# Kernel optimization log

Measured on AMD Instinct MI355X. Metric: run time of the kernel, lower is better.

The kernel has to match this reference:

```python
import jax, jax.numpy as jnp
import numpy as np

N_QUBITS = 8
HIDDEN_DIM = 128
GATE_FAMILIES = ("rx", "ry", "rz")


def _rx(theta):
    theta = jnp.asarray(theta)
    c = jnp.cos(theta / 2).astype(jnp.complex64)
    s = (-1j * jnp.sin(theta / 2)).astype(jnp.complex64)
    return jnp.stack([jnp.stack([c, s], -1), jnp.stack([s, c], -1)], -2)


def _ry(theta):
    theta = jnp.asarray(theta)
    c = jnp.cos(theta / 2).astype(jnp.complex64)
    s = jnp.sin(theta / 2).astype(jnp.complex64)
    return jnp.stack([jnp.stack([c, -s], -1), jnp.stack([s, c], -1)], -2)


def _rz(theta):
    theta = jnp.asarray(theta)
    em = jnp.exp(-0.5j * theta).astype(jnp.complex64)
    ep = jnp.exp(0.5j * theta).astype(jnp.complex64)
    z = jnp.zeros_like(em)
    return jnp.stack([jnp.stack([em, z], -1), jnp.stack([z, ep], -1)], -2)


_GATE = {"rx": _rx, "ry": _ry, "rz": _rz}


def _apply_1q(state, mat, wire, n):
    # state: (B, 2^n) complex; wire 0 is the most-significant bit (PennyLane convention)
    B = state.shape[0]
    L, R = 2 ** wire, 2 ** (n - 1 - wire)
    s = state.reshape(B, L, 2, R)
    if mat.ndim == 2:
        s = jnp.einsum("ij,bljr->blir", mat, s)
    else:  # per-sample angles -> (B,2,2) matrices
        s = jnp.einsum("bij,bljr->blir", mat, s)
    return s.reshape(B, 2 ** n)


def _apply_cnot(state, wire, n):
    # CNOT with control=wire, target=wire+1 (adjacent chain)
    B = state.shape[0]
    L, R = 2 ** wire, 2 ** (n - 2 - wire)
    s = state.reshape(B, L, 2, 2, R)
    s = jnp.concatenate([s[:, :, :1], s[:, :, 1:, ::-1]], axis=2)
    return s.reshape(B, 2 ** n)


def _circuit(x, params):
    # x: (B, n) data-encoding angles; params: (n,) trainable angles. Returns <Z_0>, shape (B,).
    B, n = x.shape
    state = jnp.zeros((B, 2 ** n), jnp.complex64).at[:, 0].set(1.0)
    for i in range(n):
        state = _apply_1q(state, _rx(x[:, i]), i, n)
    for i in range(n):
        mat = _GATE[GATE_FAMILIES[i % len(GATE_FAMILIES)]](params[i])
        state = _apply_1q(state, mat, i, n)
    for i in range(n - 1):
        state = _apply_cnot(state, i, n)
    probs = state.real ** 2 + state.imag ** 2
    p = probs.reshape(B, 2, -1).sum(-1)
    return p[:, 0] - p[:, 1]


def setup_inputs() -> dict:
    key = jax.random.key(0)
    ks = jax.random.split(key, 13)
    T, B, D, H, n = 256, 256, 128, HIDDEN_DIM, N_QUBITS
    scale = 1.0 / np.sqrt(D + H)
    inputs = jax.random.normal(ks[0], (T, B, D), jnp.float32)
    d = {"inputs": inputs}
    names = ["f", "i", "u", "o"]
    for j, nm in enumerate(names):
        d["W" + nm] = jax.random.normal(ks[1 + 3 * j], (n, D + H), jnp.float32) * scale
        d["b" + nm] = jax.random.normal(ks[2 + 3 * j], (n,), jnp.float32) * scale
        d["p" + nm] = jax.random.normal(ks[3 + 3 * j], (n,), jnp.float32)
    return d


def reference(inputs, Wf, bf, Wi, bi, Wu, bu, Wo, bo, pf, pi, pu, po):
    T, B, D = inputs.shape
    h0 = jnp.zeros((B, HIDDEN_DIM), inputs.dtype)
    c0 = jnp.zeros((B, HIDDEN_DIM), inputs.dtype)

    def step(carry, x):
        hx, cx = carry
        comb = jnp.concatenate([x, hx], axis=1)  # (B, D+H)
        f = jax.nn.sigmoid(_circuit(comb @ Wf.T + bf, pf))[:, None]
        ig = jax.nn.sigmoid(_circuit(comb @ Wi.T + bi, pi))[:, None]
        g = jnp.tanh(_circuit(comb @ Wu.T + bu, pu))[:, None]
        o = jax.nn.sigmoid(_circuit(comb @ Wo.T + bo, po))[:, None]
        cx = f * cx + ig * g
        hx = o * jnp.tanh(cx)
        return (hx, cx), hx

    (hx, cx), outs = jax.lax.scan(step, (h0, c0), inputs)
    return outs, hx, cx
```

## Files before the change

### kernel.cpp

```cpp
#include <hip/hip_runtime.h>

#define TT 256
#define BB 256
#define DD 128

__device__ __forceinline__ float rdlane(float v, int l) {
    return __int_as_float(__builtin_amdgcn_readlane(__float_as_int(v), l));
}
__device__ __forceinline__ float frcp(float x) { return __builtin_amdgcn_rcpf(x); }
__device__ __forceinline__ float fastcos(float z) {
    float r = z * 0.15915494309189535f;
    r = __builtin_amdgcn_fractf(r);
    return __builtin_amdgcn_cosf(r);
}

__global__ __launch_bounds__(256) void k_angles(
    const float* __restrict__ x,
    const float* __restrict__ Wf, const float* __restrict__ bf, const float* __restrict__ pf,
    const float* __restrict__ Wi, const float* __restrict__ bi, const float* __restrict__ pi,
    const float* __restrict__ Wu, const float* __restrict__ bu, const float* __restrict__ pu,
    const float* __restrict__ Wo, const float* __restrict__ bo, const float* __restrict__ po,
    float4* __restrict__ A)
{
    __shared__ float4 w4[4][32];
    float* w = reinterpret_cast<float*>(w4);
    int tid = threadIdx.x;
    for (int k = tid; k < 512; k += 256) {
        int g = k >> 7, j = k & 127;
        const float* W = (g == 0) ? Wf : (g == 1) ? Wi : (g == 2) ? Wu : Wo;
        w[g * 128 + j] = W[j];
    }
    __syncthreads();

    int r = blockIdx.x * 256 + tid;
    int t = r >> 8, b = r & 255;
    const float4* xr = reinterpret_cast<const float4*>(x + (size_t)r * DD);

    float af = bf[0] + pf[0];
    float ai = bi[0] + pi[0];
    float au = bu[0] + pu[0];
    float ao = bo[0] + po[0];
    #pragma unroll
    for (int k = 0; k < 32; ++k) {
        float4 v  = xr[k];
        float4 f4 = w4[0][k], i4 = w4[1][k], u4 = w4[2][k], o4 = w4[3][k];
        af = fmaf(v.x, f4.x, fmaf(v.y, f4.y, fmaf(v.z, f4.z, fmaf(v.w, f4.w, af))));
        ai = fmaf(v.x, i4.x, fmaf(v.y, i4.y, fmaf(v.z, i4.z, fmaf(v.w, i4.w, ai))));
        au = fmaf(v.x, u4.x, fmaf(v.y, u4.y, fmaf(v.z, u4.z, fmaf(v.w, u4.w, au))));
        ao = fmaf(v.x, o4.x, fmaf(v.y, o4.y, fmaf(v.z, o4.z, fmaf(v.w, o4.w, ao))));
    }
    A[b * TT + t] = make_float4(af, ai, au, ao);
}

__global__ __launch_bounds__(64) void k_recur(
    const float4* __restrict__ A,
    const float* __restrict__ Wf, const float* __restrict__ Wi,
    const float* __restrict__ Wu, const float* __restrict__ Wo,
    float* __restrict__ out)
{
    int b = blockIdx.x;
    int lane = threadIdx.x;
    __shared__ float As[4][260];

    #pragma unroll
    for (int k = 0; k < 4; ++k) {
        int t = lane + 64 * k;
        float4 a4 = A[b * TT + t];
        As[0][t] = a4.x; As[1][t] = a4.y; As[2][t] = a4.z; As[3][t] = a4.w;
    }

    int g = lane & 3;
    const float* W = (g == 0) ? Wf : (g == 1) ? Wi : (g == 2) ? Wu : Wo;
    const float4* W4 = reinterpret_cast<const float4*>(W + 128);
    float S = 0.f;
    #pragma unroll
    for (int k = 0; k < 32; ++k) {
        float4 v = W4[k];
        S += (v.x + v.y) + (v.z + v.w);
    }
    float kk   = (g == 2) ? -2.f : -1.f;
    float Aact = (g == 2) ?  2.f :  1.f;
    float Bact = (g == 2) ? -1.f :  0.f;

    __syncthreads();

    float c = 0.f, h = 0.f;
    float a_cur = As[g][0];
    float* outp = out + b * 128 + lane * 2;

    for (int t = 0; t < TT; ++t) {
        float a_next = As[g][t + 1];
        float z = fmaf(h, S, a_cur);
        float v = fastcos(z);
        float e = __expf(kk * v);
        float s = frcp(1.f + e);
        float act = fmaf(Aact, s, Bact);
        float fv = rdlane(act, 0);
        float iv = rdlane(act, 1);
        float uv = rdlane(act, 2);
        float ov = rdlane(act, 3);
        c = fmaf(fv, c, iv * uv);
        float e2 = __expf(2.f * c);
        float th = 1.f - 2.f * frcp(1.f + e2);
        h = ov * th;
        *reinterpret_cast<float2*>(outp + (size_t)t * (BB * 128)) = make_float2(h, h);
        a_cur = a_next;
    }
    float* hx = out + (size_t)TT * BB * 128;
    float* cx = hx + BB * 128;
    *reinterpret_cast<float2*>(hx + b * 128 + lane * 2) = make_float2(h, h);
    *reinterpret_cast<float2*>(cx + b * 128 + lane * 2) = make_float2(c, c);
}

extern "C" void kernel_launch(void* const* d_in, const int* in_sizes, int n_in,
                              void* d_out, int out_size, void* d_ws, size_t ws_size,
                              hipStream_t stream) {
    const float* x = (const float*)d_in[0];
    const float *Wf, *bf, *pf, *Wi, *bi, *pi, *Wu, *bu, *pu, *Wo, *bo, *po;
    if (n_in >= 13 && in_sizes[3] == 8 && in_sizes[4] == 2048) {
        Wf = (const float*)d_in[1];  bf = (const float*)d_in[2];  pf = (const float*)d_in[3];
        Wi = (const float*)d_in[4];  bi = (const float*)d_in[5];  pi = (const float*)d_in[6];
        Wu = (const float*)d_in[7];  bu = (const float*)d_in[8];  pu = (const float*)d_in[9];
        Wo = (const float*)d_in[10]; bo = (const float*)d_in[11]; po = (const float*)d_in[12];
    } else {
        Wf = (const float*)d_in[1];  bf = (const float*)d_in[2];
        Wi = (const float*)d_in[3];  bi = (const float*)d_in[4];
        Wu = (const float*)d_in[5];  bu = (const float*)d_in[6];
        Wo = (const float*)d_in[7];  bo = (const float*)d_in[8];
        pf = (const float*)d_in[9];  pi = (const float*)d_in[10];
        pu = (const float*)d_in[11]; po = (const float*)d_in[12];
    }
    float4* A = (float4*)d_ws;

    k_angles<<<dim3(256), dim3(256), 0, stream>>>(
        x, Wf, bf, pf, Wi, bi, pi, Wu, bu, pu, Wo, bo, po, A);
    k_recur<<<dim3(256), dim3(64), 0, stream>>>(
        A, Wf, Wi, Wu, Wo, (float*)d_out);
}
```

Baseline: 39.44 us.

## Run one batch row per thread in recurrence and expand outputs in separate kernel

The recurrence kernel now gives each thread a whole batch sample, computing all four gates itself instead of spreading them over four lanes and exchanging through readlane. It keeps the angle rows in a time-major layout with an 8-deep register prefetch, and writes the scalar h (and final c) back into the workspace. A new k_expand kernel then broadcasts those scalars into the full output with wide, coalesced float4 stores. The aim is to take the large strided output writes off the serial recurrence path. The cost is that only 4 blocks of 64 threads run the recurrence, so each thread carries a long dependent chain with little parallelism to hide latency.

```diff
diff --git a/kernel.cpp b/kernel.cpp
--- a/kernel.cpp
+++ b/kernel.cpp
@@ -4,15 +4,15 @@
 #define BB 256
 #define DD 128
 
-__device__ __forceinline__ float rdlane(float v, int l) {
-    return __int_as_float(__builtin_amdgcn_readlane(__float_as_int(v), l));
-}
 __device__ __forceinline__ float frcp(float x) { return __builtin_amdgcn_rcpf(x); }
 __device__ __forceinline__ float fastcos(float z) {
     float r = z * 0.15915494309189535f;
     r = __builtin_amdgcn_fractf(r);
     return __builtin_amdgcn_cosf(r);
 }
+#define C_SIG  (-1.4426950408889634f)
+#define C_TANH (-2.8853900817779268f)
+#define C_TC   ( 2.8853900817779268f)
 
 __global__ __launch_bounds__(256) void k_angles(
     const float* __restrict__ x,
@@ -33,7 +33,6 @@
     __syncthreads();
 
     int r = blockIdx.x * 256 + tid;
-    int t = r >> 8, b = r & 255;
     const float4* xr = reinterpret_cast<const float4*>(x + (size_t)r * DD);
 
     float af = bf[0] + pf[0];
@@ -49,67 +48,88 @@
         au = fmaf(v.x, u4.x, fmaf(v.y, u4.y, fmaf(v.z, u4.z, fmaf(v.w, u4.w, au))));
         ao = fmaf(v.x, o4.x, fmaf(v.y, o4.y, fmaf(v.z, o4.z, fmaf(v.w, o4.w, ao))));
     }
-    A[b * TT + t] = make_float4(af, ai, au, ao);
+    A[r] = make_float4(af, ai, au, ao);
 }
 
 __global__ __launch_bounds__(64) void k_recur(
-    const float4* __restrict__ A,
+    float4* __restrict__ A,
     const float* __restrict__ Wf, const float* __restrict__ Wi,
-    const float* __restrict__ Wu, const float* __restrict__ Wo,
-    float* __restrict__ out)
+    const float* __restrict__ Wu, const float* __restrict__ Wo)
 {
-    int b = blockIdx.x;
-    int lane = threadIdx.x;
-    __shared__ float As[4][260];
+    int bg = blockIdx.x * 64 + threadIdx.x;
 
-    #pragma unroll
-    for (int k = 0; k < 4; ++k) {
-        int t = lane + 64 * k;
-        float4 a4 = A[b * TT + t];
-        As[0][t] = a4.x; As[1][t] = a4.y; As[2][t] = a4.z; As[3][t] = a4.w;
+    float Sf = 0.f, Si = 0.f, Su = 0.f, So = 0.f;
+    {
+        const float4* F4 = reinterpret_cast<const float4*>(Wf + 128);
+        const float4* I4 = reinterpret_cast<const float4*>(Wi + 128);
+        const float4* U4 = reinterpret_cast<const float4*>(Wu + 128);
+        const float4* O4 = reinterpret_cast<const float4*>(Wo + 128);
+        #pragma unroll
+        for (int k = 0; k < 32; ++k) {
+            float4 a = F4[k], b = I4[k], c = U4[k], d = O4[k];
+            Sf += (a.x + a.y) + (a.z + a.w);
+            Si += (b.x + b.y) + (b.z + b.w);
+            Su += (c.x + c.y) + (c.z + c.w);
+            So += (d.x + d.y) + (d.z + d.w);
+        }
     }
 
-    int g = lane & 3;
-    const float* W = (g == 0) ? Wf : (g == 1) ? Wi : (g == 2) ? Wu : Wo;
-    const float4* W4 = reinterpret_cast<const float4*>(W + 128);
-    float S = 0.f;
-    #pragma unroll
-    for (int k = 0; k < 32; ++k) {
-        float4 v = W4[k];
-        S += (v.x + v.y) + (v.z + v.w);
+    float4* Ab = A + bg;
+    float c = 0.f, h = 0.f;
+
+    float4 p0 = Ab[0*BB], p1 = Ab[1*BB], p2 = Ab[2*BB], p3 = Ab[3*BB];
+    float4 p4 = Ab[4*BB], p5 = Ab[5*BB], p6 = Ab[6*BB], p7 = Ab[7*BB];
+
+#define STEP(P, TIDX)                                                        \
+    {                                                                        \
+        float zf = fmaf(h, Sf, P.x), zi = fmaf(h, Si, P.y);                  \
+        float zu = fmaf(h, Su, P.z), zo = fmaf(h, So, P.w);                  \
+        float vf = fastcos(zf), vi = fastcos(zi);                            \
+        float vu = fastcos(zu), vo = fastcos(zo);                            \
+        float ef = __builtin_amdgcn_exp2f(vf * C_SIG);                       \
+        float ei = __builtin_amdgcn_exp2f(vi * C_SIG);                       \
+        float eu = __builtin_amdgcn_exp2f(vu * C_TANH);                      \
+        float eo = __builtin_amdgcn_exp2f(vo * C_SIG);                       \
+        float fg = frcp(1.f + ef), ig = frcp(1.f + ei), og = frcp(1.f + eo); \
+        float ug = fmaf(2.f, frcp(1.f + eu), -1.f);                          \
+        c = fmaf(fg, c, ig * ug);                                            \
+        float e2 = __builtin_amdgcn_exp2f(c * C_TC);                         \
+        float th = fmaf(-2.f, frcp(1.f + e2), 1.f);                          \
+        h = og * th;                                                         \
+        reinterpret_cast<float*>(Ab + (TIDX) * BB)[0] = h;                   \
     }
-    float kk   = (g == 2) ? -2.f : -1.f;
-    float Aact = (g == 2) ?  2.f :  1.f;
-    float Bact = (g == 2) ? -1.f :  0.f;
 
-    __syncthreads();
+    for (int t = 0; t < TT; t += 8) {
+        int tn = t + 8;
+        STEP(p0, t + 0); p0 = Ab[(size_t)min(tn + 0, TT - 1) * BB];
+        STEP(p1, t + 1); p1 = Ab[(size_t)min(tn + 1, TT - 1) * BB];
+        STEP(p2, t + 2); p2 = Ab[(size_t)min(tn + 2, TT - 1) * BB];
+        STEP(p3, t + 3); p3 = Ab[(size_t)min(tn + 3, TT - 1) * BB];
+        STEP(p4, t + 4); p4 = Ab[(size_t)min(tn + 4, TT - 1) * BB];
+        STEP(p5, t + 5); p5 = Ab[(size_t)min(tn + 5, TT - 1) * BB];
+        STEP(p6, t + 6); p6 = Ab[(size_t)min(tn + 6, TT - 1) * BB];
+        STEP(p7, t + 7); p7 = Ab[(size_t)min(tn + 7, TT - 1) * BB];
+    }
+#undef STEP
+    reinterpret_cast<float*>(Ab + (TT - 1) * BB)[1] = c;
+}
 
-    float c = 0.f, h = 0.f;
-    float a_cur = As[g][0];
-    float* outp = out + b * 128 + lane * 2;
-
-    for (int t = 0; t < TT; ++t) {
-        float a_next = As[g][t + 1];
-        float z = fmaf(h, S, a_cur);
-        float v = fastcos(z);
-        float e = __expf(kk * v);
-        float s = frcp(1.f + e);
-        float act = fmaf(Aact, s, Bact);
-        float fv = rdlane(act, 0);
-        float iv = rdlane(act, 1);
-        float uv = rdlane(act, 2);
-        float ov = rdlane(act, 3);
-        c = fmaf(fv, c, iv * uv);
-        float e2 = __expf(2.f * c);
-        float th = 1.f - 2.f * frcp(1.f + e2);
-        h = ov * th;
-        *reinterpret_cast<float2*>(outp + (size_t)t * (BB * 128)) = make_float2(h, h);
-        a_cur = a_next;
+__global__ __launch_bounds__(256) void k_expand(
+    const float4* __restrict__ A, float4* __restrict__ out)
+{
+    unsigned r = blockIdx.x * 256 + threadIdx.x;
+    const unsigned OUTS4 = (unsigned)TT * BB * 128 / 4;
+    const unsigned HX4   = (unsigned)BB * 128 / 4;
+    float v;
+    if (r < OUTS4) {
+        v = A[r >> 5].x;
+    } else {
+        unsigned q = r - OUTS4;
+        unsigned b = (q & (HX4 - 1)) >> 5;
+        float4 a = A[(TT - 1) * BB + b];
+        v = (q < HX4) ? a.x : a.y;
     }
-    float* hx = out + (size_t)TT * BB * 128;
-    float* cx = hx + BB * 128;
-    *reinterpret_cast<float2*>(hx + b * 128 + lane * 2) = make_float2(h, h);
-    *reinterpret_cast<float2*>(cx + b * 128 + lane * 2) = make_float2(c, c);
+    out[r] = make_float4(v, v, v, v);
 }
 
 extern "C" void kernel_launch(void* const* d_in, const int* in_sizes, int n_in,
@@ -134,6 +154,7 @@
 
     k_angles<<<dim3(256), dim3(256), 0, stream>>>(
         x, Wf, bf, pf, Wi, bi, pi, Wu, bu, pu, Wo, bo, po, A);
-    k_recur<<<dim3(256), dim3(64), 0, stream>>>(
-        A, Wf, Wi, Wu, Wo, (float*)d_out);
+    k_recur<<<dim3(4), dim3(64), 0, stream>>>(A, Wf, Wi, Wu, Wo);
+    k_expand<<<dim3((TT * BB * 128 / 4 + 2 * BB * 128 / 4) / 256), dim3(256), 0, stream>>>(
+        A, (float4*)d_out);
 }
```

Result: slower. 58.30 us (+47.8%).
